# Kernel optimization log

Measured on AMD Instinct MI355X. Metric: run time of the kernel, lower is better.

The kernel has to match this reference:

```python
import jax, jax.numpy as jnp
import numpy as np

B, S, E, H = 4, 2048, 256, 8
DK = E // H


def setup_inputs() -> dict:
    key = jax.random.key(0)
    ks = jax.random.split(key, 12)
    glorot = lambda k, shape: jax.random.uniform(k, shape, jnp.float32, -1.0, 1.0) * jnp.sqrt(6.0 / (shape[0] + shape[1]))
    inp = {
        "q": jax.random.normal(ks[0], (B, S, E), jnp.float32),
        "k": jax.random.normal(ks[1], (B, S, E), jnp.float32),
        "v": jax.random.normal(ks[2], (B, S, E), jnp.float32),
        # causal mask, np.triu(k=1)==0 -> lower triangular including diagonal
        "mask": (jnp.triu(jnp.ones((S, S), jnp.int32), k=1) == 0).astype(jnp.int32)[None, None],
        "Wq": glorot(ks[3], (E, E)), "bq": jnp.zeros((E,), jnp.float32),
        "Wk": glorot(ks[4], (E, E)), "bk": jnp.zeros((E,), jnp.float32),
        "Wv": glorot(ks[5], (E, E)), "bv": jnp.zeros((E,), jnp.float32),
        "Wo": glorot(ks[6], (E, E)), "bo": jnp.zeros((E,), jnp.float32),
        "gammas": glorot(ks[7], (H, 1)).reshape(H, 1, 1),  # xavier init of (H,1,1)
    }
    return inp


def reference(q, k, v, mask, Wq, bq, Wk, bk, Wv, bv, Wo, bo, gammas):
    b, s, e = q.shape
    h = gammas.shape[0]
    dk = e // h
    neg = jnp.float32(-1e32)

    def proj(x, W, bias):
        return (x @ W.T + bias).reshape(b, s, h, dk).transpose(0, 2, 1, 3)  # [B,H,S,dk]

    qh, kh, vh = proj(q, Wq, bq), proj(k, Wk, bk), proj(v, Wv, bv)
    scores = jnp.einsum("bhid,bhjd->bhij", qh, kh) / jnp.sqrt(jnp.float32(dk))  # [B,H,S,S]

    # --- no_grad block: monotonic distance-decay term ---
    maskf = mask.astype(scores.dtype)
    s1 = jax.nn.softmax(jnp.where(mask == 0, neg, scores), axis=-1) * maskf
    s1 = jax.lax.stop_gradient(s1)
    distcum = jnp.cumsum(s1, axis=-1)
    disttotal = jnp.sum(s1, axis=-1, keepdims=True)
    idx = jnp.arange(s)
    pos = jnp.abs(idx[None, :] - idx[:, None]).astype(scores.dtype)[None, None]  # |i-j|
    dist = jnp.sqrt(jnp.clip((disttotal - distcum) * pos, 0.0, None))
    dist = jax.lax.stop_gradient(dist)
    # ----------------------------------------------------

    gamma = -jax.nn.softplus(gammas)[None]                      # [1,H,1,1]
    total_effect = jnp.clip(jnp.exp(dist * gamma), 1e-5, 1e5)
    scores = jnp.where(mask == 0, neg, scores * total_effect)
    attn = jax.nn.softmax(scores, axis=-1)                      # zero_pad=False (mask=1 path)
    out = jnp.einsum("bhij,bhjd->bhid", attn, vh)
    concat = out.transpose(0, 2, 1, 3).reshape(b, s, e)
    return concat @ Wo.T + bo
```

## Files before the change

### kernel.cpp

```cpp
#include <hip/hip_runtime.h>
#include <math.h>

#define B_   4
#define S_   2048
#define E_   256
#define H_   8
#define DK_  32
#define NROWS (B_*S_)

typedef unsigned short ushort_t;
typedef __attribute__((ext_vector_type(8))) short  bf16x8;
typedef __attribute__((ext_vector_type(4))) float  f32x4;

#define LOG2E 1.4426950408889634f
#define QSCALE (0.17677669529663687f * 1.4426950408889634f)

#if __has_builtin(__builtin_amdgcn_exp2f)
#define EXP2F(x) __builtin_amdgcn_exp2f(x)
#else
#define EXP2F(x) exp2f(x)
#endif
#if __has_builtin(__builtin_amdgcn_sqrtf)
#define SQRTF(x) __builtin_amdgcn_sqrtf(x)
#else
#define SQRTF(x) sqrtf(x)
#endif
#if __has_builtin(__builtin_amdgcn_rcpf)
#define RCPF(x) __builtin_amdgcn_rcpf(x)
#else
#define RCPF(x) (1.0f/(x))
#endif

__device__ __forceinline__ ushort_t bf16_rne(float x)
{
    unsigned int u = __float_as_uint(x);
    unsigned int r = u + 0x7FFFu + ((u >> 16) & 1u);
    return (ushort_t)(r >> 16);
}
__device__ __forceinline__ float bf16_to_f(ushort_t h)
{
    return __uint_as_float(((unsigned int)h) << 16);
}

__device__ __forceinline__ float scan16(float x)
{
    x += __int_as_float(__builtin_amdgcn_update_dpp(0, __float_as_int(x), 0x111, 0xF, 0xF, true));
    x += __int_as_float(__builtin_amdgcn_update_dpp(0, __float_as_int(x), 0x112, 0xF, 0xF, true));
    x += __int_as_float(__builtin_amdgcn_update_dpp(0, __float_as_int(x), 0x114, 0xF, 0xF, true));
    x += __int_as_float(__builtin_amdgcn_update_dpp(0, __float_as_int(x), 0x118, 0xF, 0xF, true));
    return x;
}
__device__ __forceinline__ float bcast15(float x)
{
    return __int_as_float(__builtin_amdgcn_ds_swizzle(__float_as_int(x), 0x1F0));
}


__global__ __launch_bounds__(256)
void conv_all(const float* __restrict__ q, const float* __restrict__ k,
              const float* __restrict__ v,
              const float* __restrict__ Wq, const float* __restrict__ Wk,
              const float* __restrict__ Wv, const float* __restrict__ Wo,
              ushort_t* __restrict__ xh, ushort_t* __restrict__ xl,
              ushort_t* __restrict__ wh, ushort_t* __restrict__ wl)
{
    const int z = blockIdx.y;
    const float* src;
    ushort_t *dh, *dl;
    if (z < 3) {
        src = (z == 0) ? q : (z == 1) ? k : v;
        dh = xh + (size_t)z * (NROWS * E_);
        dl = xl + (size_t)z * (NROWS * E_);
    } else {
        if (blockIdx.x >= 16) return;
        src = (z == 3) ? Wq : (z == 4) ? Wk : (z == 5) ? Wv : Wo;
        dh = wh + (size_t)(z - 3) * (E_ * E_);
        dl = wl + (size_t)(z - 3) * (E_ * E_);
    }
    const int n0 = blockIdx.x * 16;
    const int lr = threadIdx.x & 15, kq = threadIdx.x >> 4;
    #pragma unroll
    for (int half = 0; half < 2; half++) {
        const int kk = kq * 8 + half * 128;
        const float* s = src + (size_t)(n0 + lr) * E_ + kk;
        const float4 a = *(const float4*)s;
        const float4 b = *(const float4*)(s + 4);
        const float xs[8] = {a.x, a.y, a.z, a.w, b.x, b.y, b.z, b.w};
        bf16x8 hv, lv;
        #pragma unroll
        for (int e = 0; e < 8; e++) {
            const ushort_t hb = bf16_rne(xs[e]);
            hv[e] = (short)hb;
            lv[e] = (short)bf16_rne(xs[e] - bf16_to_f(hb));
        }
        const size_t o = ((size_t)blockIdx.x * 8 + (kk >> 5)) * 512
                       + ((kk >> 3) & 3) * 128 + lr * 8;
        *(bf16x8*)&dh[o] = hv;
        *(bf16x8*)&dl[o] = lv;
    }
}

__device__ __forceinline__ void gemm_lds_core(
    const ushort_t* __restrict__ Ah, const ushort_t* __restrict__ Al,
    const ushort_t* __restrict__ Bh, const ushort_t* __restrict__ Bl,
    int nstrip, int mb, int wv, int lane,
    ushort_t* __restrict__ sBh, ushort_t* __restrict__ sBl,
    f32x4 (&acc)[4])
{
    const size_t aoff = (size_t)nstrip * 8 * 512 + lane * 8;
    const size_t boff = (size_t)(mb * 4 + wv) * 8 * 512 + lane * 8;
    const int lw = wv * 512 + lane * 8;

    bf16x8 aH = *(const bf16x8*)(Ah + aoff);
    bf16x8 aL = *(const bf16x8*)(Al + aoff);
    {
        const bf16x8 sH = *(const bf16x8*)(Bh + boff);
        const bf16x8 sL = *(const bf16x8*)(Bl + boff);
        *(bf16x8*)&sBh[lw] = sH;
        *(bf16x8*)&sBl[lw] = sL;
    }

    #pragma unroll
    for (int kc = 0; kc < 8; kc++) {
        __syncthreads();
        const int cur = (kc & 1) * 2048;
        bf16x8 aH2, aL2, sH2, sL2;
        if (kc < 7) {
            aH2 = *(const bf16x8*)(Ah + aoff + (size_t)(kc + 1) * 512);
            aL2 = *(const bf16x8*)(Al + aoff + (size_t)(kc + 1) * 512);
            sH2 = *(const bf16x8*)(Bh + boff + (size_t)(kc + 1) * 512);
            sL2 = *(const bf16x8*)(Bl + boff + (size_t)(kc + 1) * 512);
        }
        #pragma unroll
        for (int t = 0; t < 4; t++) {
            const int ro = cur + t * 512 + lane * 8;
            const bf16x8 bH = *(const bf16x8*)&sBh[ro];
            const bf16x8 bL = *(const bf16x8*)&sBl[ro];
            acc[t] = __builtin_amdgcn_mfma_f32_16x16x32_bf16(aL, bH, acc[t], 0, 0, 0);
            acc[t] = __builtin_amdgcn_mfma_f32_16x16x32_bf16(aH, bL, acc[t], 0, 0, 0);
            acc[t] = __builtin_amdgcn_mfma_f32_16x16x32_bf16(aH, bH, acc[t], 0, 0, 0);
        }
        if (kc < 7) {
            const int nx = (cur ^ 2048) + lw;
            *(bf16x8*)&sBh[nx] = sH2;
            *(bf16x8*)&sBl[nx] = sL2;
            aH = aH2; aL = aL2;
        }
    }
}

__global__ __launch_bounds__(256)
void gemm_qkv(const ushort_t* __restrict__ Xh, const ushort_t* __restrict__ Xl,
              const ushort_t* __restrict__ Wh, const ushort_t* __restrict__ Wl,
              const float* __restrict__ bqp, const float* __restrict__ bkp,
              const float* __restrict__ bvp,
              ushort_t* __restrict__ Qh, ushort_t* __restrict__ Ql,
              ushort_t* __restrict__ Kh, ushort_t* __restrict__ Kl,
              ushort_t* __restrict__ Vt)
{
    __shared__ __align__(16) ushort_t sBh[2 * 2048];
    __shared__ __align__(16) ushort_t sBl[2 * 2048];

    const size_t N2 = (size_t)NROWS * E_;
    const size_t WN = (size_t)E_ * E_;
    const int z = blockIdx.z;
    const ushort_t* Ah = Xh + (size_t)z * N2;
    const ushort_t* Al = Xl + (size_t)z * N2;
    const ushort_t* Bh = Wh + (size_t)z * WN;
    const ushort_t* Bl = Wl + (size_t)z * WN;
    const float* bias = (z == 0) ? bqp : (z == 1) ? bkp : bvp;
    const float scale = (z == 0) ? QSCALE : 1.0f;

    const int lane = threadIdx.x & 63, wv = threadIdx.x >> 6;
    const int lr = lane & 15, lq = lane >> 4;
    const int mb = blockIdx.x;
    const int nstrip = blockIdx.y * 4 + wv;

    f32x4 acc[4] = {{0,0,0,0},{0,0,0,0},{0,0,0,0},{0,0,0,0}};
    gemm_lds_core(Ah, Al, Bh, Bl, nstrip, mb, wv, lane, sBh, sBl, acc);

    #pragma unroll
    for (int t = 0; t < 4; t++) {
        const int col = mb * 64 + t * 16 + lr;
        const float bt = bias[col];
        const int h = col >> 5, d = col & 31;
        if (z <= 1) {
            ushort_t* Y1 = (z == 0) ? Qh : Kh;
            ushort_t* Y2 = (z == 0) ? Ql : Kl;
            #pragma unroll
            for (int reg = 0; reg < 4; reg++) {
                const int n  = nstrip * 16 + lq * 4 + reg;
                const int bI = n >> 11, sI = n & (S_ - 1);
                const size_t o = (size_t)(bI * H_ + h) * (S_ * DK_)
                               + (size_t)(sI >> 4) * 512
                               + ((d >> 3) & 3) * 128 + (sI & 15) * 8 + (d & 7);
                const float y = (acc[t][reg] + bt) * scale;
                const ushort_t hb = bf16_rne(y);
                Y1[o] = hb;
                Y2[o] = bf16_rne(y - bf16_to_f(hb));
            }
        } else {
            #pragma unroll
            for (int reg = 0; reg < 4; reg++) {
                const int n  = nstrip * 16 + lq * 4 + reg;
                const int bI = n >> 11, sI = n & (S_ - 1);
                const size_t o = (size_t)(bI * H_ + h) * (S_ * DK_)
                               + (size_t)((sI >> 5) * 2 + (d >> 4)) * 512
                               + ((sI >> 3) & 3) * 128 + (d & 15) * 8 + (sI & 7);
                Vt[o] = bf16_rne(acc[t][reg] + bt);
            }
        }
    }
}

__global__ __launch_bounds__(256)
void gemm_out(const ushort_t* __restrict__ Xh, const ushort_t* __restrict__ Xl,
              const ushort_t* __restrict__ Wh, const ushort_t* __restrict__ Wl,
              const float* __restrict__ bias, float* __restrict__ Yf)
{
    __shared__ __align__(16) ushort_t sBh[2 * 2048];
    __shared__ __align__(16) ushort_t sBl[2 * 2048];

    const int lane = threadIdx.x & 63, wv = threadIdx.x >> 6;
    const int lr = lane & 15, lq = lane >> 4;
    const int mb = blockIdx.x;
    const int nstrip = blockIdx.y * 4 + wv;

    f32x4 acc[4] = {{0,0,0,0},{0,0,0,0},{0,0,0,0},{0,0,0,0}};
    gemm_lds_core(Xh, Xl, Wh, Wl, nstrip, mb, wv, lane, sBh, sBl, acc);

    #pragma unroll
    for (int t = 0; t < 4; t++) {
        const int col = mb * 64 + t * 16 + lr;
        const float bt = bias[col];
        #pragma unroll
        for (int reg = 0; reg < 4; reg++) {
            const int n = nstrip * 16 + lq * 4 + reg;
            Yf[(size_t)n * E_ + col] = acc[t][reg] + bt;
        }
    }
}

#define VPAD 72

__device__ __forceinline__ void score_tile(f32x4 (&a)[4],
    const ushort_t* __restrict__ Kbh, const ushort_t* __restrict__ Kbl,
    int jt, const bf16x8& qhi, const bf16x8& qlo, int lane, int lr, int lq,
    bool domask, int i0)
{
    #pragma unroll
    for (int tt = 0; tt < 4; tt++) {
        const size_t ko = (size_t)(jt * 4 + tt) * 512 + lane * 8;
        const bf16x8 khi = *(const bf16x8*)(Kbh + ko);
        const bf16x8 klo = *(const bf16x8*)(Kbl + ko);
        f32x4 v = {0.f, 0.f, 0.f, 0.f};
        v = __builtin_amdgcn_mfma_f32_16x16x32_bf16(qlo, khi, v, 0, 0, 0);
        v = __builtin_amdgcn_mfma_f32_16x16x32_bf16(qhi, klo, v, 0, 0, 0);
        v = __builtin_amdgcn_mfma_f32_16x16x32_bf16(qhi, khi, v, 0, 0, 0);
        a[tt] = v;
    }
    if (domask) {
        #pragma unroll
        for (int tt = 0; tt < 4; tt++)
            #pragma unroll
            for (int r = 0; r < 4; r++) {
                const int irow = i0 + lq * 4 + r;
                const int j    = jt * 64 + tt * 16 + lr;
                if (j > irow) a[tt][r] = -3.0e38f;
            }
    }
}

__global__ __launch_bounds__(256)
void attn_flash(const ushort_t* __restrict__ Qh, const ushort_t* __restrict__ Ql,
                const ushort_t* __restrict__ Kh, const ushort_t* __restrict__ Kl,
                const ushort_t* __restrict__ Vs, const float* __restrict__ gammas,
                ushort_t* __restrict__ Ch, ushort_t* __restrict__ Cl)
{
    __shared__ float sTS[16][36];
    __shared__ __align__(16) ushort_t sP[4][16 * VPAD];
    __shared__ float sO[4][16][32];
    __shared__ float sZ[4][16];

    const int tid  = threadIdx.x;
    const int lane = tid & 63, wv = tid >> 6;
    const int lr   = lane & 15, lq = lane >> 4;
    const int unit = blockIdx.x >> 7;
    const int tq   = 31 - unit;
    const int sub  = blockIdx.x & 127;
    const int bh   = sub & 31;
    const int st   = sub >> 5;
    const int h    = bh & 7, b = bh >> 3;
    const int i0   = tq * 64 + st * 16;

    const size_t hb = (size_t)bh * (S_ * DK_);
    const ushort_t* Kbh = Kh + hb;
    const ushort_t* Kbl = Kl + hb;
    const ushort_t* Vb  = Vs + hb;

    const float g   = gammas[h];
    const float gl2 = -((g > 20.f) ? g : log1pf(__expf(g))) * LOG2E;

    const size_t qoff = hb + (size_t)(i0 >> 4) * 512 + lane * 8;
    const bf16x8 qhi = *(const bf16x8*)(Qh + qoff);
    const bf16x8 qlo = *(const bf16x8*)(Ql + qoff);

    for (int jt = wv; jt <= tq; jt += 4) {
        f32x4 a[4];
        score_tile(a, Kbh, Kbl, jt, qhi, qlo, lane, lr, lq, jt == tq, i0);
        #pragma unroll
        for (int r = 0; r < 4; r++) {
            float rs = (EXP2F(a[0][r]) + EXP2F(a[1][r]))
                     + (EXP2F(a[2][r]) + EXP2F(a[3][r]));
            rs += __shfl_xor(rs, 1); rs += __shfl_xor(rs, 2);
            rs += __shfl_xor(rs, 4); rs += __shfl_xor(rs, 8);
            if (lr == 0) sTS[lq * 4 + r][jt] = rs;
        }
    }
    __syncthreads();

    float z2a[4] = {0.f, 0.f, 0.f, 0.f};
    f32x4 O0 = {0.f,0.f,0.f,0.f}, O1 = {0.f,0.f,0.f,0.f};

    if (wv <= tq) {
        float invZ[4], base[4], pr[4];
        #pragma unroll
        for (int r = 0; r < 4; r++) {
            const int row = lq * 4 + r;
            float run = 0.f, bs = 0.f;
            for (int t = 0; t <= tq; t++) {
                if (t < wv) bs += sTS[row][t];
                run += sTS[row][t];
            }
            invZ[r] = RCPF(run);
            base[r] = bs;
            pr[r]   = (float)(i0 + row - lr);
        }

        ushort_t* sPw = &sP[wv][0];
        for (int jt = wv; jt <= tq; jt += 4) {
            const int j0 = jt * 64;
            f32x4 a[4];
            score_tile(a, Kbh, Kbl, jt, qhi, qlo, lane, lr, lq, jt == tq, i0);

            float sc[4][4], tot[4][4];
            #pragma unroll
            for (int tt = 0; tt < 4; tt++)
                #pragma unroll
                for (int r = 0; r < 4; r++) {
                    const float e = EXP2F(a[tt][r]);
                    const float s = scan16(e);
                    sc[tt][r]  = s;
                    tot[tt][r] = bcast15(s);
                }
            #pragma unroll
            for (int r = 0; r < 4; r++) {
                float run2 = base[r];
                #pragma unroll
                for (int tt = 0; tt < 4; tt++) { sc[tt][r] += run2; run2 += tot[tt][r]; }
            }
            #pragma unroll
            for (int tt = 0; tt < 4; tt++) {
                const float jf = (float)(j0 + tt * 16);
                #pragma unroll
                for (int r = 0; r < 4; r++) {
                    const float rest = fmaxf(fmaf(-sc[tt][r], invZ[r], 1.0f), 0.f);
                    const float posf = pr[r] - jf;
                    const float dist = SQRTF(fmaxf(rest * posf, 0.f));
                    const float eff  = EXP2F(gl2 * dist);
                    const float p2   = EXP2F(a[tt][r] * eff);
                    z2a[r] += p2;
                    sPw[(lq * 4 + r) * VPAD + tt * 16 + lr] = bf16_rne(p2);
                }
            }
            #pragma unroll
            for (int kc = 0; kc < 2; kc++) {
                const bf16x8 pa = *(const bf16x8*)&sPw[lr * VPAD + kc * 32 + lq * 8];
                const size_t vb = (size_t)(((j0 >> 5) + kc) * 2) * 512 + lane * 8;
                const bf16x8 v0 = *(const bf16x8*)(Vb + vb);
                const bf16x8 v1 = *(const bf16x8*)(Vb + vb + 512);
                O0 = __builtin_amdgcn_mfma_f32_16x16x32_bf16(pa, v0, O0, 0, 0, 0);
                O1 = __builtin_amdgcn_mfma_f32_16x16x32_bf16(pa, v1, O1, 0, 0, 0);
            }
            if (jt + 4 <= tq) {
                #pragma unroll
                for (int r = 0; r < 4; r++) {
                    const int row = lq * 4 + r;
                    base[r] += sTS[row][jt] + sTS[row][jt+1] + sTS[row][jt+2] + sTS[row][jt+3];
                }
            }
        }
    }

    #pragma unroll
    for (int r = 0; r < 4; r++) {
        float z = z2a[r];
        z += __shfl_xor(z, 1); z += __shfl_xor(z, 2);
        z += __shfl_xor(z, 4); z += __shfl_xor(z, 8);
        if (lr == 0) sZ[wv][lq * 4 + r] = z;
        sO[wv][lq * 4 + r][lr]      = O0[r];
        sO[wv][lq * 4 + r][16 + lr] = O1[r];
    }
    __syncthreads();

    #pragma unroll
    for (int p = 0; p < 2; p++) {
        const int pid = tid + p * 256;
        const int row = pid >> 5, d = pid & 31;
        const float v = (sO[0][row][d] + sO[1][row][d]) + (sO[2][row][d] + sO[3][row][d]);
        const float z = (sZ[0][row] + sZ[1][row]) + (sZ[2][row] + sZ[3][row]);
        const float y = v * RCPF(z);
        const int nIdx = b * S_ + i0 + row;
        const size_t o = ((size_t)(nIdx >> 4) * 8 + h) * 512
                       + (d >> 3) * 128 + (nIdx & 15) * 8 + (d & 7);
        const ushort_t hbb = bf16_rne(y);
        Ch[o] = hbb;
        Cl[o] = bf16_rne(y - bf16_to_f(hbb));
    }
}

extern "C" void kernel_launch(void* const* d_in, const int* in_sizes, int n_in,
                              void* d_out, int out_size, void* d_ws, size_t ws_size,
                              hipStream_t stream)
{
    const float* q      = (const float*)d_in[0];
    const float* k      = (const float*)d_in[1];
    const float* v      = (const float*)d_in[2];
    const float* Wq     = (const float*)d_in[4];
    const float* bq     = (const float*)d_in[5];
    const float* Wk     = (const float*)d_in[6];
    const float* bk     = (const float*)d_in[7];
    const float* Wv     = (const float*)d_in[8];
    const float* bv     = (const float*)d_in[9];
    const float* Wo     = (const float*)d_in[10];
    const float* bo     = (const float*)d_in[11];
    const float* gammas = (const float*)d_in[12];
    float* out = (float*)d_out;

    const size_t N2 = (size_t)NROWS * E_;
    const size_t WN = (size_t)E_ * E_;

    ushort_t* p   = (ushort_t*)d_ws;
    ushort_t* xh  = p;
    ushort_t* xl  = xh + 3 * N2;
    ushort_t* wh  = xl + 3 * N2;
    ushort_t* wl  = wh + 4 * WN;
    ushort_t* qh  = wl + 4 * WN;
    ushort_t* ql  = qh + N2;
    ushort_t* kh  = ql + N2;
    ushort_t* kl  = kh + N2;
    ushort_t* vt  = kl + N2;
    ushort_t* ch  = xh;
    ushort_t* cl  = xh + N2;

    conv_all<<<dim3(NROWS / 16, 7), 256, 0, stream>>>(q, k, v, Wq, Wk, Wv, Wo,
                                                      xh, xl, wh, wl);

    gemm_qkv<<<dim3(E_ / 64, NROWS / 64, 3), 256, 0, stream>>>(
        xh, xl, wh, wl, bq, bk, bv, qh, ql, kh, kl, vt);

    attn_flash<<<32 * 32 * 4, 256, 0, stream>>>(qh, ql, kh, kl, vt, gammas, ch, cl);

    gemm_out<<<dim3(E_ / 64, NROWS / 64), 256, 0, stream>>>(
        ch, cl, wh + 3 * WN, wl + 3 * WN, bo, out);
}
```

Before: 237.2 us.

## Fuse fp32-to-bf16 split of activations into QKV GEMM and vectorize Q/K stores

Input activation conversion to hi/lo bf16 pairs moves out of a separate pass and into the QKV projection GEMM, which now reads fp32 q/k/v directly and splits them in registers. This removes a full write and re-read of the three converted activation tensors, but each of the 4 column blocks now converts the same rows again. The Q/K epilogue goes through shared memory so it can write 16-byte vectorized stores instead of scattered 2-byte stores. The change also drops a redundant clamp in the attention decay term and simplifies block index decoding.

```diff
diff --git a/kernel.cpp b/kernel.cpp
--- a/kernel.cpp
+++ b/kernel.cpp
@@ -57,26 +57,14 @@
 
 
 __global__ __launch_bounds__(256)
-void conv_all(const float* __restrict__ q, const float* __restrict__ k,
-              const float* __restrict__ v,
-              const float* __restrict__ Wq, const float* __restrict__ Wk,
-              const float* __restrict__ Wv, const float* __restrict__ Wo,
-              ushort_t* __restrict__ xh, ushort_t* __restrict__ xl,
-              ushort_t* __restrict__ wh, ushort_t* __restrict__ wl)
+void conv_w(const float* __restrict__ Wq, const float* __restrict__ Wk,
+            const float* __restrict__ Wv, const float* __restrict__ Wo,
+            ushort_t* __restrict__ wh, ushort_t* __restrict__ wl)
 {
     const int z = blockIdx.y;
-    const float* src;
-    ushort_t *dh, *dl;
-    if (z < 3) {
-        src = (z == 0) ? q : (z == 1) ? k : v;
-        dh = xh + (size_t)z * (NROWS * E_);
-        dl = xl + (size_t)z * (NROWS * E_);
-    } else {
-        if (blockIdx.x >= 16) return;
-        src = (z == 3) ? Wq : (z == 4) ? Wk : (z == 5) ? Wv : Wo;
-        dh = wh + (size_t)(z - 3) * (E_ * E_);
-        dl = wl + (size_t)(z - 3) * (E_ * E_);
-    }
+    const float* src = (z == 0) ? Wq : (z == 1) ? Wk : (z == 2) ? Wv : Wo;
+    ushort_t* dh = wh + (size_t)z * (E_ * E_);
+    ushort_t* dl = wl + (size_t)z * (E_ * E_);
     const int n0 = blockIdx.x * 16;
     const int lr = threadIdx.x & 15, kq = threadIdx.x >> 4;
     #pragma unroll
@@ -100,19 +88,41 @@
     }
 }
 
-__device__ __forceinline__ void gemm_lds_core(
-    const ushort_t* __restrict__ Ah, const ushort_t* __restrict__ Al,
-    const ushort_t* __restrict__ Bh, const ushort_t* __restrict__ Bl,
-    int nstrip, int mb, int wv, int lane,
-    ushort_t* __restrict__ sBh, ushort_t* __restrict__ sBl,
-    f32x4 (&acc)[4])
-{
-    const size_t aoff = (size_t)nstrip * 8 * 512 + lane * 8;
+__global__ __launch_bounds__(256)
+void gemm_qkv(const float* __restrict__ Xq, const float* __restrict__ Xk,
+              const float* __restrict__ Xv,
+              const ushort_t* __restrict__ Wh, const ushort_t* __restrict__ Wl,
+              const float* __restrict__ bqp, const float* __restrict__ bkp,
+              const float* __restrict__ bvp,
+              ushort_t* __restrict__ Qh, ushort_t* __restrict__ Ql,
+              ushort_t* __restrict__ Kh, ushort_t* __restrict__ Kl,
+              ushort_t* __restrict__ Vt)
+{
+    __shared__ __align__(16) float sF[4][16][68];
+    ushort_t* sBh = (ushort_t*)&sF[0][0][0];
+    ushort_t* sBl = sBh + 4096;
+
+    const size_t WN = (size_t)E_ * E_;
+    const int z = blockIdx.z;
+    const float* Xf = (z == 0) ? Xq : (z == 1) ? Xk : Xv;
+    const ushort_t* Bh = Wh + (size_t)z * WN;
+    const ushort_t* Bl = Wl + (size_t)z * WN;
+    const float* bias = (z == 0) ? bqp : (z == 1) ? bkp : bvp;
+    const float scale = (z == 0) ? QSCALE : 1.0f;
+
+    const int lane = threadIdx.x & 63, wv = threadIdx.x >> 6;
+    const int lr = lane & 15, lq = lane >> 4;
+    const int mb = blockIdx.x;
+    const int nstrip = blockIdx.y * 4 + wv;
+
+    const float* arow = Xf + (size_t)(nstrip * 16 + lr) * E_ + lq * 8;
     const size_t boff = (size_t)(mb * 4 + wv) * 8 * 512 + lane * 8;
     const int lw = wv * 512 + lane * 8;
 
-    bf16x8 aH = *(const bf16x8*)(Ah + aoff);
-    bf16x8 aL = *(const bf16x8*)(Al + aoff);
+    f32x4 acc[4] = {{0,0,0,0},{0,0,0,0},{0,0,0,0},{0,0,0,0}};
+
+    float4 a0 = *(const float4*)(arow);
+    float4 a1 = *(const float4*)(arow + 4);
     {
         const bf16x8 sH = *(const bf16x8*)(Bh + boff);
         const bf16x8 sL = *(const bf16x8*)(Bl + boff);
@@ -124,12 +134,22 @@
     for (int kc = 0; kc < 8; kc++) {
         __syncthreads();
         const int cur = (kc & 1) * 2048;
-        bf16x8 aH2, aL2, sH2, sL2;
+        float4 a0n, a1n; bf16x8 sH2, sL2;
         if (kc < 7) {
-            aH2 = *(const bf16x8*)(Ah + aoff + (size_t)(kc + 1) * 512);
-            aL2 = *(const bf16x8*)(Al + aoff + (size_t)(kc + 1) * 512);
+            a0n = *(const float4*)(arow + (kc + 1) * 32);
+            a1n = *(const float4*)(arow + (kc + 1) * 32 + 4);
             sH2 = *(const bf16x8*)(Bh + boff + (size_t)(kc + 1) * 512);
             sL2 = *(const bf16x8*)(Bl + boff + (size_t)(kc + 1) * 512);
+        }
+        bf16x8 aH, aL;
+        {
+            const float xs[8] = {a0.x, a0.y, a0.z, a0.w, a1.x, a1.y, a1.z, a1.w};
+            #pragma unroll
+            for (int e = 0; e < 8; e++) {
+                const ushort_t hb = bf16_rne(xs[e]);
+                aH[e] = (short)hb;
+                aL[e] = (short)bf16_rne(xs[e] - bf16_to_f(hb));
+            }
         }
         #pragma unroll
         for (int t = 0; t < 4; t++) {
@@ -144,62 +164,49 @@
             const int nx = (cur ^ 2048) + lw;
             *(bf16x8*)&sBh[nx] = sH2;
             *(bf16x8*)&sBl[nx] = sL2;
-            aH = aH2; aL = aL2;
-        }
-    }
-}
-
-__global__ __launch_bounds__(256)
-void gemm_qkv(const ushort_t* __restrict__ Xh, const ushort_t* __restrict__ Xl,
-              const ushort_t* __restrict__ Wh, const ushort_t* __restrict__ Wl,
-              const float* __restrict__ bqp, const float* __restrict__ bkp,
-              const float* __restrict__ bvp,
-              ushort_t* __restrict__ Qh, ushort_t* __restrict__ Ql,
-              ushort_t* __restrict__ Kh, ushort_t* __restrict__ Kl,
-              ushort_t* __restrict__ Vt)
-{
-    __shared__ __align__(16) ushort_t sBh[2 * 2048];
-    __shared__ __align__(16) ushort_t sBl[2 * 2048];
-
-    const size_t N2 = (size_t)NROWS * E_;
-    const size_t WN = (size_t)E_ * E_;
-    const int z = blockIdx.z;
-    const ushort_t* Ah = Xh + (size_t)z * N2;
-    const ushort_t* Al = Xl + (size_t)z * N2;
-    const ushort_t* Bh = Wh + (size_t)z * WN;
-    const ushort_t* Bl = Wl + (size_t)z * WN;
-    const float* bias = (z == 0) ? bqp : (z == 1) ? bkp : bvp;
-    const float scale = (z == 0) ? QSCALE : 1.0f;
-
-    const int lane = threadIdx.x & 63, wv = threadIdx.x >> 6;
-    const int lr = lane & 15, lq = lane >> 4;
-    const int mb = blockIdx.x;
-    const int nstrip = blockIdx.y * 4 + wv;
-
-    f32x4 acc[4] = {{0,0,0,0},{0,0,0,0},{0,0,0,0},{0,0,0,0}};
-    gemm_lds_core(Ah, Al, Bh, Bl, nstrip, mb, wv, lane, sBh, sBl, acc);
-
-    #pragma unroll
-    for (int t = 0; t < 4; t++) {
-        const int col = mb * 64 + t * 16 + lr;
-        const float bt = bias[col];
-        const int h = col >> 5, d = col & 31;
-        if (z <= 1) {
-            ushort_t* Y1 = (z == 0) ? Qh : Kh;
-            ushort_t* Y2 = (z == 0) ? Ql : Kl;
-            #pragma unroll
-            for (int reg = 0; reg < 4; reg++) {
-                const int n  = nstrip * 16 + lq * 4 + reg;
-                const int bI = n >> 11, sI = n & (S_ - 1);
-                const size_t o = (size_t)(bI * H_ + h) * (S_ * DK_)
-                               + (size_t)(sI >> 4) * 512
-                               + ((d >> 3) & 3) * 128 + (sI & 15) * 8 + (d & 7);
-                const float y = (acc[t][reg] + bt) * scale;
-                const ushort_t hb = bf16_rne(y);
-                Y1[o] = hb;
-                Y2[o] = bf16_rne(y - bf16_to_f(hb));
-            }
-        } else {
+            a0 = a0n; a1 = a1n;
+        }
+    }
+    __syncthreads();
+
+    if (z <= 1) {
+        #pragma unroll
+        for (int t = 0; t < 4; t++) {
+            const float bt = bias[mb * 64 + t * 16 + lr];
+            #pragma unroll
+            for (int reg = 0; reg < 4; reg++)
+                sF[wv][lq * 4 + reg][t * 16 + lr] = (acc[t][reg] + bt) * scale;
+        }
+        ushort_t* Y1 = z ? Kh : Qh;
+        ushort_t* Y2 = z ? Kl : Ql;
+        const int bI   = nstrip >> 7;
+        const int sblk = nstrip & 127;
+        const int qg = lane >> 4, s = lane & 15;
+        #pragma unroll
+        for (int cg = 0; cg < 2; cg++) {
+            const float* src = &sF[wv][s][cg * 32 + qg * 8];
+            const float4 v0 = *(const float4*)src;
+            const float4 v1 = *(const float4*)(src + 4);
+            const float xs[8] = {v0.x, v0.y, v0.z, v0.w, v1.x, v1.y, v1.z, v1.w};
+            bf16x8 hv, lv;
+            #pragma unroll
+            for (int e = 0; e < 8; e++) {
+                const ushort_t hb = bf16_rne(xs[e]);
+                hv[e] = (short)hb;
+                lv[e] = (short)bf16_rne(xs[e] - bf16_to_f(hb));
+            }
+            const int h = mb * 2 + cg;
+            const size_t o = (size_t)(bI * H_ + h) * (S_ * DK_)
+                           + (size_t)sblk * 512 + lane * 8;
+            *(bf16x8*)&Y1[o] = hv;
+            *(bf16x8*)&Y2[o] = lv;
+        }
+    } else {
+        #pragma unroll
+        for (int t = 0; t < 4; t++) {
+            const int col = mb * 64 + t * 16 + lr;
+            const float bt = bias[col];
+            const int h = col >> 5, d = col & 31;
             #pragma unroll
             for (int reg = 0; reg < 4; reg++) {
                 const int n  = nstrip * 16 + lq * 4 + reg;
@@ -226,8 +233,48 @@
     const int mb = blockIdx.x;
     const int nstrip = blockIdx.y * 4 + wv;
 
+    const size_t aoff = (size_t)nstrip * 8 * 512 + lane * 8;
+    const size_t boff = (size_t)(mb * 4 + wv) * 8 * 512 + lane * 8;
+    const int lw = wv * 512 + lane * 8;
+
     f32x4 acc[4] = {{0,0,0,0},{0,0,0,0},{0,0,0,0},{0,0,0,0}};
-    gemm_lds_core(Xh, Xl, Wh, Wl, nstrip, mb, wv, lane, sBh, sBl, acc);
+
+    bf16x8 aH = *(const bf16x8*)(Xh + aoff);
+    bf16x8 aL = *(const bf16x8*)(Xl + aoff);
+    {
+        const bf16x8 sH = *(const bf16x8*)(Wh + boff);
+        const bf16x8 sL = *(const bf16x8*)(Wl + boff);
+        *(bf16x8*)&sBh[lw] = sH;
+        *(bf16x8*)&sBl[lw] = sL;
+    }
+
+    #pragma unroll
+    for (int kc = 0; kc < 8; kc++) {
+        __syncthreads();
+        const int cur = (kc & 1) * 2048;
+        bf16x8 aH2, aL2, sH2, sL2;
+        if (kc < 7) {
+            aH2 = *(const bf16x8*)(Xh + aoff + (size_t)(kc + 1) * 512);
+            aL2 = *(const bf16x8*)(Xl + aoff + (size_t)(kc + 1) * 512);
+            sH2 = *(const bf16x8*)(Wh + boff + (size_t)(kc + 1) * 512);
+            sL2 = *(const bf16x8*)(Wl + boff + (size_t)(kc + 1) * 512);
+        }
+        #pragma unroll
+        for (int t = 0; t < 4; t++) {
+            const int ro = cur + t * 512 + lane * 8;
+            const bf16x8 bH = *(const bf16x8*)&sBh[ro];
+            const bf16x8 bL = *(const bf16x8*)&sBl[ro];
+            acc[t] = __builtin_amdgcn_mfma_f32_16x16x32_bf16(aL, bH, acc[t], 0, 0, 0);
+            acc[t] = __builtin_amdgcn_mfma_f32_16x16x32_bf16(aH, bL, acc[t], 0, 0, 0);
+            acc[t] = __builtin_amdgcn_mfma_f32_16x16x32_bf16(aH, bH, acc[t], 0, 0, 0);
+        }
+        if (kc < 7) {
+            const int nx = (cur ^ 2048) + lw;
+            *(bf16x8*)&sBh[nx] = sH2;
+            *(bf16x8*)&sBl[nx] = sL2;
+            aH = aH2; aL = aL2;
+        }
+    }
 
     #pragma unroll
     for (int t = 0; t < 4; t++) {
@@ -285,11 +332,9 @@
     const int tid  = threadIdx.x;
     const int lane = tid & 63, wv = tid >> 6;
     const int lr   = lane & 15, lq = lane >> 4;
-    const int unit = blockIdx.x >> 7;
-    const int tq   = 31 - unit;
-    const int sub  = blockIdx.x & 127;
-    const int bh   = sub & 31;
-    const int st   = sub >> 5;
+    const int bh   = blockIdx.x & 31;
+    const int st   = (blockIdx.x >> 5) & 3;
+    const int tq   = 31 - (blockIdx.x >> 7);
     const int h    = bh & 7, b = bh >> 3;
     const int i0   = tq * 64 + st * 16;
 
@@ -364,7 +409,7 @@
                 const float jf = (float)(j0 + tt * 16);
                 #pragma unroll
                 for (int r = 0; r < 4; r++) {
-                    const float rest = fmaxf(fmaf(-sc[tt][r], invZ[r], 1.0f), 0.f);
+                    const float rest = fmaf(-sc[tt][r], invZ[r], 1.0f);
                     const float posf = pr[r] - jf;
                     const float dist = SQRTF(fmaxf(rest * posf, 0.f));
                     const float eff  = EXP2F(gl2 * dist);
@@ -440,24 +485,20 @@
     const size_t N2 = (size_t)NROWS * E_;
     const size_t WN = (size_t)E_ * E_;
 
-    ushort_t* p   = (ushort_t*)d_ws;
-    ushort_t* xh  = p;
-    ushort_t* xl  = xh + 3 * N2;
-    ushort_t* wh  = xl + 3 * N2;
-    ushort_t* wl  = wh + 4 * WN;
-    ushort_t* qh  = wl + 4 * WN;
-    ushort_t* ql  = qh + N2;
-    ushort_t* kh  = ql + N2;
-    ushort_t* kl  = kh + N2;
-    ushort_t* vt  = kl + N2;
-    ushort_t* ch  = xh;
-    ushort_t* cl  = xh + N2;
-
-    conv_all<<<dim3(NROWS / 16, 7), 256, 0, stream>>>(q, k, v, Wq, Wk, Wv, Wo,
-                                                      xh, xl, wh, wl);
+    ushort_t* wh = (ushort_t*)d_ws;
+    ushort_t* wl = wh + 4 * WN;
+    ushort_t* qh = wl + 4 * WN;
+    ushort_t* ql = qh + N2;
+    ushort_t* kh = ql + N2;
+    ushort_t* kl = kh + N2;
+    ushort_t* vt = kl + N2;
+    ushort_t* ch = vt + N2;
+    ushort_t* cl = ch + N2;
+
+    conv_w<<<dim3(16, 4), 256, 0, stream>>>(Wq, Wk, Wv, Wo, wh, wl);
 
     gemm_qkv<<<dim3(E_ / 64, NROWS / 64, 3), 256, 0, stream>>>(
-        xh, xl, wh, wl, bq, bk, bv, qh, ql, kh, kl, vt);
+        q, k, v, wh, wl, bq, bk, bv, qh, ql, kh, kl, vt);
 
     attn_flash<<<32 * 32 * 4, 256, 0, stream>>>(qh, ql, kh, kl, vt, gammas, ch, cl);
 
```

New measurement: 230.0 us. -3.0%, faster.
